# Kernel optimization log

Measured on AMD Instinct MI355X. Metric: run time of the kernel, lower is better.

Reference implementation:

```python
import jax, jax.numpy as jnp
import numpy as np

HEADS = 8
DIM = 512
DHEAD = DIM // HEADS          # 64
M_LAND = DIM // 2             # 256 landmarks
PINV_ITERS = 6
RES_K = 33                    # residual depthwise conv kernel along sequence


def _ln(x, w, b, eps=1e-5):
    mu = x.mean(-1, keepdims=True)
    var = ((x - mu) ** 2).mean(-1, keepdims=True)
    return (x - mu) * jax.lax.rsqrt(var + eps) * w + b


def _moore_penrose_pinv(x, iters=PINV_ITERS):
    # x: [b, h, m, m]; iterative Newton-Schulz style pseudo-inverse (order-3)
    abs_x = jnp.abs(x)
    col = abs_x.sum(-1).max()   # global max, matching torch.max(col)
    row = abs_x.sum(-2).max()
    z = jnp.swapaxes(x, -1, -2) / (col * row)
    I = jnp.eye(x.shape[-1], dtype=x.dtype)
    for _ in range(iters):
        xz = x @ z
        z = 0.25 * (z @ (13.0 * I - xz @ (15.0 * I - xz @ (7.0 * I - xz))))
    return z


def _nystrom_attention(x, qkv_w, out_w, out_b, res_w):
    # x: [b, n, dim]; pads at FRONT to multiple of num_landmarks
    b, n, _ = x.shape
    m = M_LAND
    pad = (m - n % m) % m
    xp = jnp.pad(x, ((0, 0), (pad, 0), (0, 0)))
    npad = n + pad
    qkv = xp @ qkv_w.T                               # [b, npad, 3*dim], no bias
    q, k, v = jnp.split(qkv, 3, axis=-1)
    heads = lambda t: t.reshape(b, npad, HEADS, DHEAD).transpose(0, 2, 1, 3)
    q, k, v = heads(q), heads(k), heads(v)           # [b, h, npad, d]
    q = q * (DHEAD ** -0.5)
    l = npad // m                                    # group size per landmark
    q_l = q.reshape(b, HEADS, m, l, DHEAD).sum(3) / l  # [b, h, m, d]
    k_l = k.reshape(b, HEADS, m, l, DHEAD).sum(3) / l
    attn1 = jax.nn.softmax(jnp.einsum('bhid,bhjd->bhij', q, k_l), -1)    # [b,h,npad,m]
    attn2 = jax.nn.softmax(jnp.einsum('bhid,bhjd->bhij', q_l, k_l), -1)  # [b,h,m,m]
    attn3 = jax.nn.softmax(jnp.einsum('bhid,bhjd->bhij', q_l, k), -1)    # [b,h,m,npad]
    attn2_inv = _moore_penrose_pinv(attn2)
    out = attn1 @ (attn2_inv @ (attn3 @ v))          # [b, h, npad, d]
    # residual depthwise conv along sequence axis (heads as channels)
    res = jax.lax.conv_general_dilated(
        v, res_w, (1, 1), ((RES_K // 2, RES_K // 2), (0, 0)),
        feature_group_count=HEADS,
        dimension_numbers=('NCHW', 'OIHW', 'NCHW'))
    out = out + res
    out = out.transpose(0, 2, 1, 3).reshape(b, npad, HEADS * DHEAD)
    out = out @ out_w.T + out_b                      # dropout = eval no-op
    return out[:, -n:]


def _translayer(x, nw, nb, qkv_w, out_w, out_b, res_w):
    return x + _nystrom_attention(_ln(x, nw, nb), qkv_w, out_w, out_b, res_w)


def _dwconv(feat, w, b, k):
    y = jax.lax.conv_general_dilated(
        feat, w, (1, 1), ((k // 2, k // 2), (k // 2, k // 2)),
        feature_group_count=DIM,
        dimension_numbers=('NCHW', 'OIHW', 'NCHW'))
    return y + b[None, :, None, None]


def _ppeg(x, w7, b7, w5, b5, w3, b3):
    B, N, C = x.shape
    H = int(np.ceil(np.sqrt(N)))   # static (N is static under jit)
    add = H * H - N
    if add > 0:
        x = jnp.concatenate([x, x[:, :add]], 1)
    feat = jnp.swapaxes(x, 1, 2).reshape(B, C, H, H)
    out = feat + _dwconv(feat, w7, b7, 7) + _dwconv(feat, w5, b5, 5) + _dwconv(feat, w3, b3, 3)
    x = jnp.swapaxes(out.reshape(B, C, H * H), 1, 2)
    if add > 0:
        x = x[:, :-add]
    return x


def setup_inputs() -> dict:
    key = jax.random.key(0)
    ks = jax.random.split(key, 24)
    B, N, C = 2, 8192, DIM
    g = lambda k, shape, s=0.02: jax.random.normal(k, shape, jnp.float32) * s
    d = {}
    d['x'] = jax.random.normal(ks[0], (B, N, C), jnp.float32)
    d['cls_token'] = jax.random.normal(ks[1], (1, 1, C), jnp.float32)
    for li, off in (('l1', 2), ('l2', 8)):
        d[li + '_norm_w'] = jnp.ones((C,), jnp.float32)
        d[li + '_norm_b'] = jnp.zeros((C,), jnp.float32)
        d[li + '_qkv_w'] = g(ks[off], (3 * C, C))
        d[li + '_out_w'] = g(ks[off + 1], (C, C))
        d[li + '_out_b'] = jnp.zeros((C,), jnp.float32)
        d[li + '_res_w'] = g(ks[off + 2], (HEADS, 1, RES_K, 1))
    d['peg_w7'] = g(ks[14], (C, 1, 7, 7)); d['peg_b7'] = jnp.zeros((C,), jnp.float32)
    d['peg_w5'] = g(ks[15], (C, 1, 5, 5)); d['peg_b5'] = jnp.zeros((C,), jnp.float32)
    d['peg_w3'] = g(ks[16], (C, 1, 3, 3)); d['peg_b3'] = jnp.zeros((C,), jnp.float32)
    d['norm_w'] = jnp.ones((C,), jnp.float32)
    d['norm_b'] = jnp.zeros((C,), jnp.float32)
    return d


def reference(x, cls_token,
              l1_norm_w, l1_norm_b, l1_qkv_w, l1_out_w, l1_out_b, l1_res_w,
              l2_norm_w, l2_norm_b, l2_qkv_w, l2_out_w, l2_out_b, l2_res_w,
              peg_w7, peg_b7, peg_w5, peg_b5, peg_w3, peg_b3,
              norm_w, norm_b):
    B = x.shape[0]
    cls = jnp.broadcast_to(cls_token, (B, 1, DIM))
    h = jnp.concatenate([cls, x], 1)
    h = _translayer(h, l1_norm_w, l1_norm_b, l1_qkv_w, l1_out_w, l1_out_b, l1_res_w)
    patches = _ppeg(h[:, 1:], peg_w7, peg_b7, peg_w5, peg_b5, peg_w3, peg_b3)
    h = jnp.concatenate([h[:, :1], patches], 1)
    h = _translayer(h, l2_norm_w, l2_norm_b, l2_qkv_w, l2_out_w, l2_out_b, l2_res_w)
    h = _ln(h, norm_w, norm_b)
    return h[:, 0]
```

## Files before the change

### kernel.cpp

```cpp
#include <hip/hip_runtime.h>
#include <hip/hip_bf16.h>

using bf16 = __hip_bfloat16;
typedef unsigned short u16;
typedef short bf16x8 __attribute__((ext_vector_type(8)));
typedef float f32x4 __attribute__((ext_vector_type(4)));

constexpr int BB    = 2;
constexpr int NSEQ  = 8193;
constexpr int CDIM  = 512;
constexpr int NH    = 8;
constexpr int DHD   = 64;
constexpr int ML    = 256;
constexpr int LF    = 33;
constexpr int NPAD  = 8448;
constexpr int PADL  = 255;
constexpr int ROWS  = BB * NSEQ;
constexpr int BH    = BB * NH;
constexpr int RKS   = 33;
constexpr int HG    = 91;
constexpr int HW2   = HG * HG;
constexpr int NPATCH = 8192;
constexpr long SQ   = (long)ML * ML;

__device__ __forceinline__ float b2f(u16 u) {
  union { unsigned int i; float f; } x; x.i = (unsigned int)u << 16; return x.f;
}
__device__ __forceinline__ short f2b(float f) {
  __hip_bfloat16 h = __float2bfloat16(f);
  return *reinterpret_cast<short*>(&h);
}
__device__ __forceinline__ f32x4 mfma16(bf16x8 a, bf16x8 b, f32x4 c) {
  return __builtin_amdgcn_mfma_f32_16x16x32_bf16(a, b, c, 0, 0, 0);
}


__global__ __launch_bounds__(256) void k_build_h(
    const float* __restrict__ x, const float* __restrict__ cls, float* __restrict__ h)
{
  long idx = (long)blockIdx.x * 256 + threadIdx.x;
  if (idx >= (long)ROWS * CDIM) return;
  int c = idx & 511;
  long r = idx >> 9;
  int b = (int)(r / NSEQ), i = (int)(r % NSEQ);
  h[idx] = (i == 0) ? cls[c] : x[((long)b * (NSEQ - 1) + (i - 1)) * CDIM + c];
}

__global__ __launch_bounds__(256) void k_cvt(
    const float* __restrict__ X, short* __restrict__ Y, long n)
{
  long i = (long)blockIdx.x * 256 + threadIdx.x;
  const long st = (long)gridDim.x * 256;
  for (; i < n; i += st) Y[i] = f2b(X[i]);
}

__global__ __launch_bounds__(256) void k_zpad(uint4* __restrict__ q)
{
  const int seg = blockIdx.y;
  const int buf = seg >> 4, bh = seg & 15;
  const long base_e = ((long)buf * BH + bh) * ((long)NPAD * DHD);
  uint4* p = (uint4*)((u16*)q + base_e);
  const int n16 = PADL * DHD * 2 / 16;
  for (int i = blockIdx.x * 256 + threadIdx.x; i < n16; i += gridDim.x * 256)
    p[i] = make_uint4(0u, 0u, 0u, 0u);
}

__global__ __launch_bounds__(256) void k_lnq(
    const float* __restrict__ X, const float* __restrict__ g,
    const float* __restrict__ bb, bf16* __restrict__ Y)
{
  __shared__ float red[4];
  const long row = blockIdx.x;
  const float* x = X + row * CDIM;
  const int t = threadIdx.x;
  float a0 = x[t], a1 = x[t + 256];
  float s = a0 + a1;
  for (int o = 32; o; o >>= 1) s += __shfl_down(s, o);
  if ((t & 63) == 0) red[t >> 6] = s;
  __syncthreads();
  const float mu = (red[0] + red[1] + red[2] + red[3]) * (1.0f / CDIM);
  __syncthreads();
  float d0 = a0 - mu, d1 = a1 - mu;
  float q = d0 * d0 + d1 * d1;
  for (int o = 32; o; o >>= 1) q += __shfl_down(q, o);
  if ((t & 63) == 0) red[t >> 6] = q;
  __syncthreads();
  const float var = (red[0] + red[1] + red[2] + red[3]) * (1.0f / CDIM);
  const float rs = rsqrtf(var + 1e-5f);
  u16* y = (u16*)Y + row * CDIM;
  y[t]       = (u16)f2b(d0 * rs * g[t]       + bb[t]);
  y[t + 256] = (u16)f2b(d1 * rs * g[t + 256] + bb[t + 256]);
}

__global__ __launch_bounds__(256) void k_final_ln(
    const float* __restrict__ H, const float* __restrict__ g,
    const float* __restrict__ bb, float* __restrict__ out)
{
  __shared__ float red[4];
  const float* x = H + (long)blockIdx.x * NSEQ * CDIM;
  const int t = threadIdx.x;
  float a0 = x[t], a1 = x[t + 256];
  float s = a0 + a1;
  for (int o = 32; o; o >>= 1) s += __shfl_down(s, o);
  if ((t & 63) == 0) red[t >> 6] = s;
  __syncthreads();
  const float mu = (red[0] + red[1] + red[2] + red[3]) * (1.0f / CDIM);
// ... 52 lines not shown
  const int t = threadIdx.x;
  float rs = 0.f, cs = 0.f;
  for (int j = 0; j < ML; ++j) { rs += fabsf(Ab[t * ML + j]); cs += fabsf(Ab[j * ML + t]); }
  for (int o = 32; o; o >>= 1) { rs = fmaxf(rs, __shfl_down(rs, o)); cs = fmaxf(cs, __shfl_down(cs, o)); }
  if ((t & 63) == 0) { r1[t >> 6] = rs; r2[t >> 6] = cs; }
  __syncthreads();
  if (t == 0) {
    red[blockIdx.x]      = fmaxf(fmaxf(r1[0], r1[1]), fmaxf(r1[2], r1[3]));
    red[16 + blockIdx.x] = fmaxf(fmaxf(r2[0], r2[1]), fmaxf(r2[2], r2[3]));
  }
}

__global__ void k_pinv_scale(float* __restrict__ red)
{
  if (threadIdx.x == 0 && blockIdx.x == 0) {
    float cmax = red[0], rmax = red[16];
    for (int i = 1; i < 16; ++i) { cmax = fmaxf(cmax, red[i]); rmax = fmaxf(rmax, red[16 + i]); }
    red[32] = 1.0f / (cmax * rmax);
  }
}

__global__ __launch_bounds__(256) void k_tscale2(
    const float* __restrict__ A, const float* __restrict__ red,
    short* __restrict__ Ab, short* __restrict__ Z, short* __restrict__ Zt)
{
  long idx = (long)blockIdx.x * 256 + threadIdx.x;
  if (idx >= (long)BH * SQ) return;
  int c = idx & 255, r = (int)((idx >> 8) & 255);
  long bh = idx >> 16;
  float a = A[idx];
  float s = red[32];
  Ab[idx] = f2b(a);
  Zt[idx] = f2b(a * s);
  Z[(bh << 16) + ((long)c << 8) + r] = f2b(a * s);
}

__global__ __launch_bounds__(256) void k_split(
    const float* __restrict__ X, float alpha, float diag,
    short* __restrict__ rH, short* __restrict__ rL,
    short* __restrict__ cH, short* __restrict__ cL)
{
  long idx = (long)blockIdx.x * 256 + threadIdx.x;
  if (idx >= (long)BH * SQ) return;
  int c = idx & 255, r = (int)((idx >> 8) & 255);
  long bh = idx >> 16;
  float v = alpha * X[idx] + ((r == c) ? diag : 0.f);
  short h = f2b(v);
  short lo = f2b(v - b2f((u16)h));
  if (rH) { rH[idx] = h; rL[idx] = lo; }
  if (cH) { long tix = (bh << 16) + ((long)c << 8) + r; cH[tix] = h; cL[tix] = lo; }
}

__global__ __launch_bounds__(256) void k_resconv2(
    const bf16* __restrict__ v, const float* __restrict__ w, bf16* __restrict__ out)
{
  __shared__ u16 vb[96][64];
  __shared__ float ws[RKS];
  const int bh = blockIdx.y, i0 = blockIdx.x * 64;
  const int t = threadIdx.x;
  if (t < RKS) ws[t] = w[(bh & 7) * RKS + t];
  const u16* vsrc = (const u16*)v + (long)bh * NPAD * DHD;
#pragma unroll
  for (int i = 0; i < 3; ++i) {
    int chunk = t + 256 * i;
    int row = chunk >> 3, c8 = (chunk & 7) * 8;
    int vrow = i0 - 16 + row;
    bf16x8 val;
    if (vrow >= 0 && vrow < NPAD) val = *(const bf16x8*)(vsrc + (long)vrow * DHD + c8);
    else { for (int j = 0; j < 8; ++j) val[j] = 0; }
    *(bf16x8*)(&vb[row][c8]) = val;
  }
  __syncthreads();
  const int d = t & 63;
  u16* ob = (u16*)out + ((long)bh * NPAD + i0) * DHD;
#pragma unroll
  for (int j = 0; j < 16; ++j) {
    int r = (t >> 6) + j * 4;
    float s = 0.f;
#pragma unroll
    for (int k = 0; k < RKS; ++k) s += b2f(vb[r + k][d]) * ws[k];
    long oi = (long)r * DHD + d;
    ob[oi] = (u16)f2b(b2f(ob[oi]) + s);
  }
}

__global__ __launch_bounds__(256) void k_vT(const bf16* __restrict__ V, bf16* __restrict__ VT)
{
  __shared__ u16 tl[64][72];
  const int r0 = blockIdx.x * 64, bh = blockIdx.y;
  const u16* vp = (const u16*)V + ((long)bh * NPAD + r0) * DHD;
  const int t = threadIdx.x;
  {
    int r = t >> 2, c0 = (t & 3) * 16;
    bf16x8 u0 = *(const bf16x8*)(vp + (long)r * DHD + c0);
    bf16x8 u1 = *(const bf16x8*)(vp + (long)r * DHD + c0 + 8);
#pragma unroll
    for (int i = 0; i < 8; ++i) { tl[r][c0 + i] = (u16)u0[i]; tl[r][c0 + 8 + i] = (u16)u1[i]; }
  }
  __syncthreads();
  {
    int d = t >> 2, k0 = (t & 3) * 16;
    bf16x8 u0, u1;
#pragma unroll
    for (int i = 0; i < 8; ++i) { u0[i] = (short)tl[k0 + i][d]; u1[i] = (short)tl[k0 + 8 + i][d]; }
    u16* dst = (u16*)VT + ((long)bh * DHD + d) * NPAD + r0 + k0;
    *(bf16x8*)dst = u0;
    *(bf16x8*)(dst + 8) = u1;
  }
}

__global__ __launch_bounds__(256) void k_t2mT(const float* __restrict__ T2M, short* __restrict__ T2MT)
{
  int idx = blockIdx.x * 256 + threadIdx.x;
  if (idx >= BH * DHD * ML) return;
  int k = idx & 255, d = (idx >> 8) & 63, bh = idx >> 14;
  T2MT[idx] = f2b(T2M[((long)bh * ML + k) * DHD + d]);
}


__global__ __launch_bounds__(256) void k_ppeg_build_t(
    const float* __restrict__ h, float* __restrict__ feat)
{
  __shared__ float tile[32][33];
  const int c0 = blockIdx.x * 32;
  const int p0 = blockIdx.y * 32;
  const int b  = blockIdx.z;
  const int t = threadIdx.x;
  const int tc = t & 31, tr8 = t >> 5;
  const int srcb = (p0 >= NPATCH) ? p0 - NPATCH : p0;
#pragma unroll
  for (int i = 0; i < 4; ++i) {
    int pp = tr8 + i * 8;
    if (p0 + pp < HW2)
      tile[pp][tc] = h[((long)b * NSEQ + 1 + srcb + pp) * CDIM + c0 + tc];
  }
  __syncthreads();
#pragma unroll
  for (int i = 0; i < 4; ++i) {
    int cc = tr8 + i * 8;
    if (p0 + tc < HW2)
      feat[((long)(b * CDIM + c0 + cc)) * HW2 + p0 + tc] = tile[tc][cc];
  }
}

__global__ __launch_bounds__(256) void k_ppeg_conv2(
    const float* __restrict__ feat,
    const float* __restrict__ w7, const float* __restrict__ b7,
    const float* __restrict__ w5, const float* __restrict__ b5,
    const float* __restrict__ w3, const float* __restrict__ b3,
    float* __restrict__ ofeat)
{
  __shared__ float P[97 * 97];
  __shared__ float ws[84];
  const int bx = blockIdx.x;
  const int c = bx & 511;
  const int t = threadIdx.x;
  for (int i = t; i < 97 * 97; i += 256) P[i] = 0.f;
  if (t < 49) ws[t] = w7[c * 49 + t];
  else if (t < 74) ws[t] = w5[c * 25 + (t - 49)];
  else if (t < 83) ws[t] = w3[c * 9 + (t - 74)];
  __syncthreads();
  const float* fp = feat + (long)bx * HW2;
  for (int i = t; i < HW2; i += 256) {
    int y = i / HG, x = i - y * HG;
    P[(y + 3) * 97 + x + 3] = fp[i];
  }
// ... 168 lines not shown
        u16* dst = (u16*)(which == 0 ? Q : (which == 1 ? Kp : V));
        dst[(((long)(b * NH + hd)) * NPAD + PADL + ii) * DHD + d] = (u16)f2b(val);
      }
    }
  }
}

__global__ __launch_bounds__(256) void k_mfma_out2(
    const bf16* __restrict__ O1, const short* __restrict__ Wm,
    const float* __restrict__ bias, float* __restrict__ Hh)
{
  __shared__ __align__(16) short As[128 * 32];
  __shared__ __align__(16) short Bs[128 * 32];
  const int m0 = blockIdx.x * 128, n0 = blockIdx.y * 128;
  const int t = threadIdx.x, w = t >> 6, l = t & 63;
  const int srow = t >> 1, skh = (t & 1) * 16;
  const int aR = m0 + srow;
  int bb = 0, ii = 0;
  if (aR < ROWS) { bb = aR / NSEQ; ii = aR - bb * NSEQ; }
  const int wR = n0 + srow;
  const int g0 = skh >> 3;
  const int sw0 = ((g0 ^ (srow & 3)) << 3), sw1 = (((g0 + 1) ^ (srow & 3)) << 3);
  const u16* o1 = (const u16*)O1;
  f32x4 acc[4][4] = {};
  for (int kt = 0; kt < 16; ++kt) {
    const int kbase = kt * 32 + skh;
    {
      bf16x8 v0, v1;
      if (aR < ROWS) {
        int hd = kbase >> 6, d0 = kbase & 63;
        const u16* src = o1 + (((long)(bb * NH + hd)) * NPAD + PADL + ii) * DHD + d0;
        v0 = *(const bf16x8*)src;
        v1 = *(const bf16x8*)(src + 8);
      } else {
#pragma unroll
        for (int i = 0; i < 8; ++i) { v0[i] = 0; v1[i] = 0; }
      }
      *(bf16x8*)(As + srow * 32 + sw0) = v0;
      *(bf16x8*)(As + srow * 32 + sw1) = v1;
    }
    {
      bf16x8 v0 = *(const bf16x8*)(Wm + (long)wR * CDIM + kbase);
      bf16x8 v1 = *(const bf16x8*)(Wm + (long)wR * CDIM + kbase + 8);
      *(bf16x8*)(Bs + srow * 32 + sw0) = v0;
      *(bf16x8*)(Bs + srow * 32 + sw1) = v1;
    }
    __syncthreads();
    const int ar0 = (w >> 1) * 64, bc0 = (w & 1) * 64;
    const int kg = l >> 4;
    bf16x8 a[4], b[4];
#pragma unroll
    for (int am = 0; am < 4; ++am) {
      int row = ar0 + am * 16 + (l & 15);
      a[am] = *(const bf16x8*)(As + row * 32 + ((kg ^ (row & 3)) << 3));
    }
#pragma unroll
    for (int bn = 0; bn < 4; ++bn) {
      int row = bc0 + bn * 16 + (l & 15);
      b[bn] = *(const bf16x8*)(Bs + row * 32 + ((kg ^ (row & 3)) << 3));
    }
#pragma unroll
    for (int am = 0; am < 4; ++am)
#pragma unroll
      for (int bn = 0; bn < 4; ++bn) acc[am][bn] = mfma16(a[am], b[bn], acc[am][bn]);
    __syncthreads();
  }
  const int ar0 = (w >> 1) * 64, bc0 = (w & 1) * 64;
#pragma unroll
  for (int am = 0; am < 4; ++am) {
#pragma unroll
    for (int rr = 0; rr < 4; ++rr) {
      int R = m0 + ar0 + am * 16 + ((l >> 4) << 2) + rr;
      if (R >= ROWS) continue;
      float* hrow = Hh + (long)R * CDIM;
#pragma unroll
      for (int bn = 0; bn < 4; ++bn) {
        int n = n0 + bc0 + bn * 16 + (l & 15);
        hrow[n] += acc[am][bn][rr] + bias[n];
      }
    }
  }
}


__global__ __launch_bounds__(256) void k_pinv_g(
    const short* __restrict__ A, const short* __restrict__ Bt,
    short* __restrict__ outN, float aN, float dN,
    short* __restrict__ outT, float aT, float dT,
    float* __restrict__ outF, float aF)
{
  const int bh = blockIdx.z;
  const long off = (long)bh * SQ;
  const short* Ab = A + off;
  const short* Btb = Bt + off;
  const int t = threadIdx.x, w = t >> 6, l = t & 63;
  const int r0 = blockIdx.x * 64 + (w >> 1) * 32;
  const int c0 = blockIdx.y * 64 + (w & 1) * 32;
  f32x4 acc[2][2] = {};
#pragma unroll
  for (int ks = 0; ks < 8; ++ks) {
    bf16x8 a[2], b[2];
#pragma unroll
    for (int am = 0; am < 2; ++am)
      a[am] = *(const bf16x8*)(Ab + (long)(r0 + am * 16 + (l & 15)) * ML + ks * 32 + (l >> 4) * 8);
#pragma unroll
    for (int bn = 0; bn < 2; ++bn)
      b[bn] = *(const bf16x8*)(Btb + (long)(c0 + bn * 16 + (l & 15)) * ML + ks * 32 + (l >> 4) * 8);
#pragma unroll
    for (int am = 0; am < 2; ++am)
#pragma unroll
      for (int bn = 0; bn < 2; ++bn) acc[am][bn] = mfma16(a[am], b[bn], acc[am][bn]);
  }
#pragma unroll
  for (int am = 0; am < 2; ++am)
#pragma unroll
    for (int bn = 0; bn < 2; ++bn)
#pragma unroll
      for (int rr = 0; rr < 4; ++rr) {
        int R = r0 + am * 16 + ((l >> 4) << 2) + rr;
        int C = c0 + bn * 16 + (l & 15);
        float x = acc[am][bn][rr];
        float dg = (R == C) ? 1.f : 0.f;
        if (outN) outN[off + (long)R * ML + C] = f2b(aN * x + dN * dg);
        if (outT) outT[off + (long)C * ML + R] = f2b(aT * x + dT * dg);
        if (outF) outF[off + (long)R * ML + C] = aF * x;
      }
}

__global__ __launch_bounds__(256) void k_pinv_gs(
    const short* __restrict__ Ah, const short* __restrict__ Al,
    const short* __restrict__ BhT, const short* __restrict__ BlT,
    float* __restrict__ outF, float alpha, float diag)
{
  const int bh = blockIdx.z;
  const long off = (long)bh * SQ;
  const int t = threadIdx.x, w = t >> 6, l = t & 63;
  const int r0 = blockIdx.x * 64 + (w >> 1) * 32;
  const int c0 = blockIdx.y * 64 + (w & 1) * 32;
  f32x4 acc[2][2] = {};
#pragma unroll
  for (int ks = 0; ks < 8; ++ks) {
    bf16x8 ah[2], al[2], bh_[2], bl[2];
#pragma unroll
    for (int am = 0; am < 2; ++am) {
      long base = off + (long)(r0 + am * 16 + (l & 15)) * ML + ks * 32 + (l >> 4) * 8;
      ah[am] = *(const bf16x8*)(Ah + base);
      al[am] = *(const bf16x8*)(Al + base);
    }
#pragma unroll
    for (int bn = 0; bn < 2; ++bn) {
      long base = off + (long)(c0 + bn * 16 + (l & 15)) * ML + ks * 32 + (l >> 4) * 8;
      bh_[bn] = *(const bf16x8*)(BhT + base);
      bl[bn] = *(const bf16x8*)(BlT + base);
    }
#pragma unroll
    for (int am = 0; am < 2; ++am)
#pragma unroll
      for (int bn = 0; bn < 2; ++bn) {
        acc[am][bn] = mfma16(ah[am], bh_[bn], acc[am][bn]);
        acc[am][bn] = mfma16(ah[am], bl[bn], acc[am][bn]);
        acc[am][bn] = mfma16(al[am], bh_[bn], acc[am][bn]);
      }
  }
#pragma unroll
  for (int am = 0; am < 2; ++am)
#pragma unroll
    for (int bn = 0; bn < 2; ++bn)
#pragma unroll
      for (int rr = 0; rr < 4; ++rr) {
        int R = r0 + am * 16 + ((l >> 4) << 2) + rr;
        int C = c0 + bn * 16 + (l & 15);
        float y = alpha * acc[am][bn][rr];
        if (R == C) y += diag;
        outF[off + (long)R * ML + C] = y;
      }
}

__global__ __launch_bounds__(256) void k_score_g(
    const bf16* __restrict__ A, const bf16* __restrict__ Bt, float* __restrict__ C)
{
  const int bh = blockIdx.z;
  const u16* Ab = (const u16*)A + (long)bh * ML * DHD;
  const u16* Btb = (const u16*)Bt + (long)bh * ML * DHD;
  float* Cb = C + (long)bh * SQ;
  const int t = threadIdx.x, w = t >> 6, l = t & 63;
  const int r0 = blockIdx.x * 64 + (w >> 1) * 32;
  const int c0 = blockIdx.y * 64 + (w & 1) * 32;
  f32x4 acc[2][2] = {};
#pragma unroll
  for (int ks = 0; ks < 2; ++ks) {
    bf16x8 a[2], b[2];
#pragma unroll
    for (int am = 0; am < 2; ++am)
      a[am] = *(const bf16x8*)(Ab + (long)(r0 + am * 16 + (l & 15)) * DHD + ks * 32 + (l >> 4) * 8);
#pragma unroll
    for (int bn = 0; bn < 2; ++bn)
      b[bn] = *(const bf16x8*)(Btb + (long)(c0 + bn * 16 + (l & 15)) * DHD + ks * 32 + (l >> 4) * 8);
#pragma unroll
    for (int am = 0; am < 2; ++am)
#pragma unroll
      for (int bn = 0; bn < 2; ++bn) acc[am][bn] = mfma16(a[am], b[bn], acc[am][bn]);
  }
#pragma unroll
  for (int am = 0; am < 2; ++am)
#pragma unroll
    for (int bn = 0; bn < 2; ++bn)
#pragma unroll
      for (int rr = 0; rr < 4; ++rr) {
        int R = r0 + am * 16 + ((l >> 4) << 2) + rr;
        int Cc = c0 + bn * 16 + (l & 15);
        Cb[(long)R * ML + Cc] = acc[am][bn][rr];
      }
}


__device__ __forceinline__ int pswz(int row, int col) {
  return row * 256 + ((((col >> 3) ^ (row & 7)) << 3) | (col & 7));
}

__global__ __launch_bounds__(256) void k_attn3(
    const bf16* __restrict__ QL, const bf16* __restrict__ Kb,
    const bf16* __restrict__ VT, float* __restrict__ T3V)
{
  __shared__ __align__(16) u16 Pl[64 * 256];
  __shared__ float psum[4][64];
  __shared__ float lsum[64];
  const int bh = blockIdx.y;
  const int m0 = blockIdx.x * 64;
  const int t = threadIdx.x, w = t >> 6, l = t & 63;
  const u16* qlp = (const u16*)QL + (long)bh * ML * DHD;
  const u16* kp  = (const u16*)Kb + (long)bh * NPAD * DHD;
  const u16* vtp = (const u16*)VT + (long)bh * DHD * NPAD;

  bf16x8 a[4][2];
#pragma unroll
  for (int am = 0; am < 4; ++am)
#pragma unroll
    for (int ks = 0; ks < 2; ++ks)
      a[am][ks] = *(const bf16x8*)(qlp + (long)(m0 + am * 16 + (l & 15)) * DHD + ks * 32 + (l >> 4) * 8);

  float p_[16];
#pragma unroll
  for (int i = 0; i < 16; ++i) p_[i] = 0.f;
  f32x4 o[4][4] = {};

  for (int kt = 0; kt < NPAD / 256; ++kt) {
    const int kv0 = kt * 256 + w * 64;
    f32x4 s[4][4] = {};
#pragma unroll
    for (int ks = 0; ks < 2; ++ks)
#pragma unroll
      for (int bc = 0; bc < 4; ++bc) {
        bf16x8 bbv = *(const bf16x8*)(kp + (long)(kv0 + bc * 16 + (l & 15)) * DHD + ks * 32 + (l >> 4) * 8);
#pragma unroll
        for (int am = 0; am < 4; ++am) s[am][bc] = mfma16(a[am][ks], bbv, s[am][bc]);
      }
#pragma unroll
    for (int am = 0; am < 4; ++am)
#pragma unroll
      for (int bc = 0; bc < 4; ++bc)
#pragma unroll
        for (int rr = 0; rr < 4; ++rr) {
          float e = __expf(s[am][bc][rr]);
          p_[am * 4 + rr] += e;
          Pl[pswz(am * 16 + ((l >> 4) << 2) + rr, w * 64 + bc * 16 + (l & 15))] = (u16)f2b(e);
        }
    __syncthreads();
#pragma unroll
    for (int ks = 0; ks < 2; ++ks) {
      bf16x8 pa[4];
#pragma unroll
      for (int am = 0; am < 4; ++am)
        pa[am] = *(const bf16x8*)(Pl + pswz(am * 16 + (l & 15), w * 64 + ks * 32 + (l >> 4) * 8));
#pragma unroll
      for (int dn = 0; dn < 4; ++dn) {
        bf16x8 vb = *(const bf16x8*)(vtp + (long)(dn * 16 + (l & 15)) * NPAD + kt * 256 + w * 64 + ks * 32 + (l >> 4) * 8);
#pragma unroll
        for (int am = 0; am < 4; ++am) o[am][dn] = mfma16(pa[am], vb, o[am][dn]);
      }
    }
    __syncthreads();
  }
#pragma unroll
  for (int i = 0; i < 16; ++i) {
    float v = p_[i];
    v += __shfl_xor(v, 1); v += __shfl_xor(v, 2); v += __shfl_xor(v, 4); v += __shfl_xor(v, 8);
    p_[i] = v;
  }
  if ((l & 15) == 0) {
#pragma unroll
    for (int am = 0; am < 4; ++am)
#pragma unroll
      for (int rr = 0; rr < 4; ++rr)
        psum[w][am * 16 + ((l >> 4) << 2) + rr] = p_[am * 4 + rr];
  }
  __syncthreads();
  if (t < 64) lsum[t] = psum[0][t] + psum[1][t] + psum[2][t] + psum[3][t];
  __syncthreads();

  float* Obuf = (float*)Pl;
  for (int wv = 0; wv < 4; ++wv) {
    if (w == wv) {
#pragma unroll
      for (int am = 0; am < 4; ++am)
#pragma unroll
        for (int dn = 0; dn < 4; ++dn)
#pragma unroll
          for (int rr = 0; rr < 4; ++rr) {
            int row = am * 16 + ((l >> 4) << 2) + rr, col = dn * 16 + (l & 15);
            if (wv == 0) Obuf[row * 64 + col] = o[am][dn][rr];
            else         Obuf[row * 64 + col] += o[am][dn][rr];
          }
    }
    __syncthreads();
  }
  {
    int row = t >> 2, c0 = (t & 3) * 16;
    float inv = 1.0f / lsum[row];
    float* dst = T3V + ((long)bh * ML + m0 + row) * DHD + c0;
#pragma unroll
    for (int i = 0; i < 16; ++i) dst[i] = Obuf[row * 64 + c0 + i] * inv;
  }
}

__global__ __launch_bounds__(256) void k_attn1(
    const bf16* __restrict__ Qb, const bf16* __restrict__ KL,
    const short* __restrict__ T2MT, bf16* __restrict__ O1)
{
  __shared__ __align__(16) u16 Pl[64 * 256];
  __shared__ float psum[4][64];
  __shared__ float lsum[64];
  const int bh = blockIdx.y;
  const int m0 = blockIdx.x * 64;
  const int t = threadIdx.x, w = t >> 6, l = t & 63;
  const u16* qp  = (const u16*)Qb + (long)bh * NPAD * DHD;
  const u16* klp = (const u16*)KL + (long)bh * ML * DHD;
  const short* tp = T2MT + (long)bh * DHD * ML;

  bf16x8 a[4][2];
#pragma unroll
  for (int am = 0; am < 4; ++am)
#pragma unroll
    for (int ks = 0; ks < 2; ++ks)
      a[am][ks] = *(const bf16x8*)(qp + (long)(m0 + am * 16 + (l & 15)) * DHD + ks * 32 + (l >> 4) * 8);

  f32x4 s[4][4] = {};
#pragma unroll
  for (int ks = 0; ks < 2; ++ks)
#pragma unroll
    for (int bc = 0; bc < 4; ++bc) {
      bf16x8 bbv = *(const bf16x8*)(klp + (long)(w * 64 + bc * 16 + (l & 15)) * DHD + ks * 32 + (l >> 4) * 8);
#pragma unroll
      for (int am = 0; am < 4; ++am) s[am][bc] = mfma16(a[am][ks], bbv, s[am][bc]);
    }
  float p_[16];
#pragma unroll
  for (int am = 0; am < 4; ++am)
#pragma unroll
    for (int rr = 0; rr < 4; ++rr)
      p_[am * 4 + rr] = __expf(s[am][0][rr]) + __expf(s[am][1][rr])
                      + __expf(s[am][2][rr]) + __expf(s[am][3][rr]);
#pragma unroll
  for (int i = 0; i < 16; ++i) {
    float v = p_[i];
    v += __shfl_xor(v, 1); v += __shfl_xor(v, 2); v += __shfl_xor(v, 4); v += __shfl_xor(v, 8);
    p_[i] = v;
  }
  if ((l & 15) == 0) {
#pragma unroll
    for (int am = 0; am < 4; ++am)
#pragma unroll
      for (int rr = 0; rr < 4; ++rr)
        psum[w][am * 16 + ((l >> 4) << 2) + rr] = p_[am * 4 + rr];
  }
#pragma unroll
  for (int am = 0; am < 4; ++am)
#pragma unroll
    for (int bc = 0; bc < 4; ++bc)
#pragma unroll
      for (int rr = 0; rr < 4; ++rr)
        Pl[pswz(am * 16 + ((l >> 4) << 2) + rr, w * 64 + bc * 16 + (l & 15))] =
            (u16)f2b(__expf(s[am][bc][rr]));
  __syncthreads();
  if (t < 64) lsum[t] = psum[0][t] + psum[1][t] + psum[2][t] + psum[3][t];
  __syncthreads();

  f32x4 o[4][4] = {};
#pragma unroll
  for (int ks = 0; ks < 2; ++ks) {
    bf16x8 pa[4];
#pragma unroll
    for (int am = 0; am < 4; ++am)
      pa[am] = *(const bf16x8*)(Pl + pswz(am * 16 + (l & 15), w * 64 + ks * 32 + (l >> 4) * 8));
#pragma unroll
    for (int dn = 0; dn < 4; ++dn) {
      bf16x8 vb = *(const bf16x8*)((const u16*)tp + (long)(dn * 16 + (l & 15)) * ML + w * 64 + ks * 32 + (l >> 4) * 8);
#pragma unroll
      for (int am = 0; am < 4; ++am) o[am][dn] = mfma16(pa[am], vb, o[am][dn]);
    }
  }
  float* Obuf = (float*)Pl;
  __syncthreads();
  for (int wv = 0; wv < 4; ++wv) {
    if (w == wv) {
#pragma unroll
      for (int am = 0; am < 4; ++am)
#pragma unroll
        for (int dn = 0; dn < 4; ++dn)
#pragma unroll
          for (int rr = 0; rr < 4; ++rr) {
            int row = am * 16 + ((l >> 4) << 2) + rr, col = dn * 16 + (l & 15);
            if (wv == 0) Obuf[row * 64 + col] = o[am][dn][rr];
            else         Obuf[row * 64 + col] += o[am][dn][rr];
          }
    }
    __syncthreads();
  }
  {
    int row = t >> 2, c0 = (t & 3) * 16;
    float inv = 1.0f / lsum[row];
    u16* dst = (u16*)O1 + ((long)bh * NPAD + m0 + row) * DHD + c0;
    bf16x8 r0, r1;
#pragma unroll
    for (int i = 0; i < 8; ++i) {
      r0[i] = f2b(Obuf[row * 64 + c0 + i] * inv);
      r1[i] = f2b(Obuf[row * 64 + c0 + 8 + i] * inv);
    }
    *(bf16x8*)dst = r0;
    *(bf16x8*)(dst + 8) = r1;
  }
}


struct WSP {
  float *h, *a2, *Za, *t3v, *t2m, *red;
  bf16 *q, *k, *v, *vT, *ql, *kl, *lnq;
  short *pu, *wqb, *wob, *t2mT;
  short *Ab, *Zc, *Zt, *Z2, *Z2t, *xz, *w1t, *w2t;
};

static void run_translayer(const float* nw, const float* nb, const float* qkvw,
                           const float* outw, const float* outb, const float* resw,
                           WSP& w, hipStream_t s)
{
  const size_t S2 = (size_t)BH * SQ;
  short* U = w.pu;

  k_cvt<<<768, 256, 0, s>>>(qkvw, w.wqb, (long)3 * CDIM * CDIM);
  k_cvt<<<256, 256, 0, s>>>(outw, w.wob, (long)CDIM * CDIM);
  k_lnq<<<ROWS, 256, 0, s>>>(w.h, nw, nb, w.lnq);
  k_zpad<<<dim3(8, 48), 256, 0, s>>>((uint4*)w.q);
  k_mfma_qkv2<<<dim3(129, 12), 256, 0, s>>>(w.lnq, w.wqb, w.q, w.k, w.v);
  k_vT<<<dim3(NPAD / 64, BH), 256, 0, s>>>(w.v, w.vT);

  const int lmN = BH * ML * DHD;
  k_landmark<<<(lmN + 255) / 256, 256, 0, s>>>(w.q, w.ql);
  k_landmark<<<(lmN + 255) / 256, 256, 0, s>>>(w.k, w.kl);

  k_score_g<<<dim3(4, 4, BH), 256, 0, s>>>(w.ql, w.kl, w.a2);
  k_softmax<<<BH * ML, 256, 0, s>>>(w.a2, ML);
  k_pinv_prep<<<BH, 256, 0, s>>>(w.a2, w.red);
  k_pinv_scale<<<1, 64, 0, s>>>(w.red);

  k_attn3<<<dim3(4, BH), 256, 0, s>>>(w.ql, w.k, w.vT, w.t3v);

  const long nz = (long)BH * SQ;
  const int sg = (int)((nz + 255) / 256);
  k_tscale2<<<sg, 256, 0, s>>>(w.a2, w.red, w.Ab, w.Zc, w.Zt);
  short *Zc = w.Zc, *Zt = w.Zt, *Z2 = w.Z2, *Z2t = w.Z2t;
  for (int it = 0; it < 5; ++it) {
    k_pinv_g<<<dim3(4, 4, BH), 256, 0, s>>>(w.Ab, Zt, w.xz, 1.f, 0.f, w.w1t, -1.f, 7.f, nullptr, 0.f);
    k_pinv_g<<<dim3(4, 4, BH), 256, 0, s>>>(w.xz, w.w1t, nullptr, 0.f, 0.f, w.w2t, -1.f, 15.f, nullptr, 0.f);
    k_pinv_g<<<dim3(4, 4, BH), 256, 0, s>>>(w.xz, w.w2t, nullptr, 0.f, 0.f, w.w1t, -1.f, 13.f, nullptr, 0.f);
    k_pinv_g<<<dim3(4, 4, BH), 256, 0, s>>>(Zc, w.w1t, Z2, 0.25f, 0.f, Z2t, 0.25f, 0.f,
                                            (it == 4) ? w.Za : nullptr, 0.25f);
    short* tm;
    tm = Zc; Zc = Z2; Z2 = tm;
    tm = Zt; Zt = Z2t; Z2t = tm;
  }
  float* T0f = (float*)(U + 4 * S2);
  float* Tf2 = (float*)(U + 2 * S2);
  k_split<<<sg, 256, 0, s>>>(w.a2, 1.f, 0.f, U + 0 * S2, U + 1 * S2, nullptr, nullptr);
  k_split<<<sg, 256, 0, s>>>(w.Za, 1.f, 0.f, nullptr, nullptr, U + 2 * S2, U + 3 * S2);
  k_pinv_gs<<<dim3(4, 4, BH), 256, 0, s>>>(U + 0 * S2, U + 1 * S2, U + 2 * S2, U + 3 * S2, T0f, 1.f, 0.f);
  k_split<<<sg, 256, 0, s>>>(T0f, -1.f, 7.f, nullptr, nullptr, U + 6 * S2, U + 7 * S2);
  k_split<<<sg, 256, 0, s>>>(T0f, 1.f, 0.f, U + 0 * S2, U + 1 * S2, nullptr, nullptr);
  k_pinv_gs<<<dim3(4, 4, BH), 256, 0, s>>>(U + 0 * S2, U + 1 * S2, U + 6 * S2, U + 7 * S2, Tf2, 1.f, 0.f);
  k_split<<<sg, 256, 0, s>>>(Tf2, -1.f, 15.f, nullptr, nullptr, U + 6 * S2, U + 7 * S2);
  k_pinv_gs<<<dim3(4, 4, BH), 256, 0, s>>>(U + 0 * S2, U + 1 * S2, U + 6 * S2, U + 7 * S2, Tf2, 1.f, 0.f);
  k_split<<<sg, 256, 0, s>>>(Tf2, -1.f, 13.f, nullptr, nullptr, U + 4 * S2, U + 5 * S2);
  k_split<<<sg, 256, 0, s>>>(w.Za, 1.f, 0.f, U + 6 * S2, U + 7 * S2, nullptr, nullptr);
  k_pinv_gs<<<dim3(4, 4, BH), 256, 0, s>>>(U + 6 * S2, U + 7 * S2, U + 4 * S2, U + 5 * S2, w.Za, 0.25f, 0.f);

  k_gemm_nn<<<dim3(4, 1, BH), 256, 0, s>>>(w.Za, w.t3v, w.t2m, ML, DHD, ML,
                                           SQ, (long)ML * DHD, (long)ML * DHD, 1.f, 0.f);
  k_t2mT<<<(BH * DHD * ML + 255) / 256, 256, 0, s>>>(w.t2m, w.t2mT);

  k_attn1<<<dim3(NPAD / 64, BH), 256, 0, s>>>(w.q, w.kl, w.t2mT, w.q);

  k_resconv2<<<dim3(NPAD / 64, BH), 256, 0, s>>>(w.v, resw, w.q);

  k_mfma_out2<<<dim3(129, 4), 256, 0, s>>>(w.q, w.wob, outb, w.h);
}

extern "C" void kernel_launch(void* const* d_in, const int* in_sizes, int n_in,
                              void* d_out, int out_size, void* d_ws, size_t ws_size,
                              hipStream_t stream)
{
  const float* x      = (const float*)d_in[0];
  const float* cls    = (const float*)d_in[1];
  const float* l1nw   = (const float*)d_in[2];
  const float* l1nb   = (const float*)d_in[3];
  const float* l1qkvw = (const float*)d_in[4];
  const float* l1outw = (const float*)d_in[5];
  const float* l1outb = (const float*)d_in[6];
  const float* l1resw = (const float*)d_in[7];
  const float* l2nw   = (const float*)d_in[8];
  const float* l2nb   = (const float*)d_in[9];
  const float* l2qkvw = (const float*)d_in[10];
  const float* l2outw = (const float*)d_in[11];
  const float* l2outb = (const float*)d_in[12];
  const float* l2resw = (const float*)d_in[13];
  const float* pw7    = (const float*)d_in[14];
  const float* pb7    = (const float*)d_in[15];
  const float* pw5    = (const float*)d_in[16];
  const float* pb5    = (const float*)d_in[17];
  const float* pw3    = (const float*)d_in[18];
  const float* pb3    = (const float*)d_in[19];
  const float* fnw    = (const float*)d_in[20];
  const float* fnb    = (const float*)d_in[21];
  (void)in_sizes; (void)n_in; (void)out_size; (void)ws_size;

  float* W = (float*)d_ws;
  size_t o = 0;
  auto alloc = [&](size_t n) { float* p = W + o; o += n; return p; };
  WSP w;
  w.h = alloc((size_t)ROWS * CDIM);
  float* qkvr = alloc((size_t)3 * BH * NPAD * DHD / 2);
  w.q = (bf16*)qkvr;
  w.k = w.q + (size_t)BH * NPAD * DHD;
  w.v = w.k + (size_t)BH * NPAD * DHD;
  float* vtr = alloc((size_t)BH * NPAD * DHD / 2);
  w.vT  = (bf16*)vtr;
  w.lnq = (bf16*)vtr;
  w.pu  = (short*)vtr;
  {
    const size_t S2 = (size_t)BH * SQ;
    w.Ab = w.pu;             w.Zc  = w.pu + S2;     w.Zt  = w.pu + 2 * S2; w.Z2 = w.pu + 3 * S2;
    w.Z2t = w.pu + 4 * S2;   w.xz  = w.pu + 5 * S2; w.w1t = w.pu + 6 * S2; w.w2t = w.pu + 7 * S2;
  }
  float* wbr = alloc((size_t)(3 * CDIM * CDIM + CDIM * CDIM) / 2);
  w.wqb = (short*)wbr;
  w.wob = w.wqb + (size_t)3 * CDIM * CDIM;
  float* lmr = alloc((size_t)2 * BH * ML * DHD / 2);
  w.ql = (bf16*)lmr;
  w.kl = w.ql + (size_t)BH * ML * DHD;
  w.a2  = alloc((size_t)BH * SQ);
  w.Za  = alloc((size_t)BH * SQ);
  w.t3v = alloc((size_t)BH * ML * DHD);
  w.t2m = alloc((size_t)BH * ML * DHD);
  float* ttr = alloc((size_t)BH * ML * DHD / 2);
  w.t2mT = (short*)ttr;
  w.red = alloc(64);

  const long nh = (long)ROWS * CDIM;
  k_build_h<<<(int)((nh + 255) / 256), 256, 0, stream>>>(x, cls, w.h);

  run_translayer(l1nw, l1nb, l1qkvw, l1outw, l1outb, l1resw, w, stream);

  float* feat  = (float*)w.q;
  float* ofeat = (float*)w.v;
  k_ppeg_build_t<<<dim3(16, 259, BB), 256, 0, stream>>>(w.h, feat);
  k_ppeg_conv2<<<BB * CDIM, 256, 0, stream>>>(feat, pw7, pb7, pw5, pb5, pw3, pb3, ofeat);
  k_ppeg_scat_t<<<dim3(16, 256, BB), 256, 0, stream>>>(ofeat, w.h);

  run_translayer(l2nw, l2nb, l2qkvw, l2outw, l2outb, l2resw, w, stream);

  k_final_ln<<<BB, 256, 0, stream>>>(w.h, fnw, fnb, (float*)d_out);
}
```

Before: 1.712 ms.

## Split-K attn3 across sequence and compute only the cls row in layer two

The attn3 landmark-to-sequence attention is split across four sequence chunks with more, smaller blocks, and a separate reduction kernel combines the partial outputs and sums. This raises parallelism beyond the previous 64 blocks. In the second transformer layer only the cls row's output is needed for the final result, so attn1, the residual conv and the output projection are replaced by single-row kernels. This skips most of the full-sequence work and is valid because only h[:,0] is returned. The cost is extra scratch traffic for the partials, which reuse the Za buffer.

```diff
diff --git a/kernel.cpp b/kernel.cpp
--- a/kernel.cpp
+++ b/kernel.cpp
@@ -22,6 +22,8 @@
 constexpr int HW2   = HG * HG;
 constexpr int NPATCH = 8192;
 constexpr long SQ   = (long)ML * ML;
+constexpr int KSPLIT = 4;
+constexpr int NKT   = NPAD / 256;
 
 __device__ __forceinline__ float b2f(u16 u) {
   union { unsigned int i; float f; } x; x.i = (unsigned int)u << 16; return x.f;
@@ -240,6 +242,24 @@
     long oi = (long)r * DHD + d;
     ob[oi] = (u16)f2b(b2f(ob[oi]) + s);
   }
+}
+
+__global__ __launch_bounds__(256) void k_resconv_r0(
+    const bf16* __restrict__ v, const float* __restrict__ w, bf16* __restrict__ out)
+{
+  int idx = blockIdx.x * 256 + threadIdx.x;
+  if (idx >= BH * DHD) return;
+  int bh = idx >> 6, d = idx & 63;
+  const float* wp = w + (bh & 7) * RKS;
+  const u16* vb = (const u16*)v + (long)bh * NPAD * DHD + d;
+  float s = 0.f;
+#pragma unroll
+  for (int t = 0; t < RKS; ++t) {
+    int src = PADL + t - 16;
+    s += b2f(vb[(long)src * DHD]) * wp[t];
+  }
+  u16* ob = (u16*)out + ((long)bh * NPAD + PADL) * DHD + d;
+  *ob = (u16)f2b(b2f(*ob) + s);
 }
 
 __global__ __launch_bounds__(256) void k_vT(const bf16* __restrict__ V, bf16* __restrict__ VT)
@@ -574,6 +594,23 @@
   }
 }
 
+__global__ __launch_bounds__(256) void k_out_r0(
+    const bf16* __restrict__ O1, const short* __restrict__ Wm,
+    const float* __restrict__ bias, float* __restrict__ Hh)
+{
+  __shared__ float mrow[CDIM];
+  const int b = blockIdx.x, t = threadIdx.x;
+  for (int c = t; c < CDIM; c += 256)
+    mrow[c] = b2f(((const u16*)O1)[(((long)(b * NH + (c >> 6))) * NPAD + PADL) * DHD + (c & 63)]);
+  __syncthreads();
+  for (int n = t; n < CDIM; n += 256) {
+    float s = 0.f;
+    const u16* wr = (const u16*)Wm + (long)n * CDIM;
+    for (int k = 0; k < CDIM; ++k) s += mrow[k] * b2f(wr[k]);
+    Hh[(long)b * NSEQ * CDIM + n] += s + bias[n];
+  }
+}
+
 
 __global__ __launch_bounds__(256) void k_pinv_g(
     const short* __restrict__ A, const short* __restrict__ Bt,
@@ -710,91 +747,93 @@
   return row * 256 + ((((col >> 3) ^ (row & 7)) << 3) | (col & 7));
 }
 
-__global__ __launch_bounds__(256) void k_attn3(
+__global__ __launch_bounds__(256) void k_attn3s(
     const bf16* __restrict__ QL, const bf16* __restrict__ Kb,
-    const bf16* __restrict__ VT, float* __restrict__ T3V)
-{
-  __shared__ __align__(16) u16 Pl[64 * 256];
-  __shared__ float psum[4][64];
-  __shared__ float lsum[64];
-  const int bh = blockIdx.y;
-  const int m0 = blockIdx.x * 64;
+    const bf16* __restrict__ VT, float* __restrict__ po, float* __restrict__ pl)
+{
+  __shared__ __align__(16) u16 Pl[32 * 256];
+  __shared__ float psum[4][32];
+  __shared__ float lsum[32];
+  const int bh = blockIdx.z;
+  const int m0 = blockIdx.x * 32;
+  const int s  = blockIdx.y;
+  const int kt0 = (NKT * s) / KSPLIT, kt1 = (NKT * (s + 1)) / KSPLIT;
   const int t = threadIdx.x, w = t >> 6, l = t & 63;
   const u16* qlp = (const u16*)QL + (long)bh * ML * DHD;
   const u16* kp  = (const u16*)Kb + (long)bh * NPAD * DHD;
   const u16* vtp = (const u16*)VT + (long)bh * DHD * NPAD;
 
-  bf16x8 a[4][2];
-#pragma unroll
-  for (int am = 0; am < 4; ++am)
+  bf16x8 a[2][2];
+#pragma unroll
+  for (int am = 0; am < 2; ++am)
 #pragma unroll
     for (int ks = 0; ks < 2; ++ks)
       a[am][ks] = *(const bf16x8*)(qlp + (long)(m0 + am * 16 + (l & 15)) * DHD + ks * 32 + (l >> 4) * 8);
 
-  float p_[16];
-#pragma unroll
-  for (int i = 0; i < 16; ++i) p_[i] = 0.f;
-  f32x4 o[4][4] = {};
-
-  for (int kt = 0; kt < NPAD / 256; ++kt) {
+  float p_[8];
+#pragma unroll
+  for (int i = 0; i < 8; ++i) p_[i] = 0.f;
+  f32x4 o[2][4] = {};
+
+  for (int kt = kt0; kt < kt1; ++kt) {
     const int kv0 = kt * 256 + w * 64;
-    f32x4 s[4][4] = {};
+    f32x4 sa[2][4] = {};
 #pragma unroll
     for (int ks = 0; ks < 2; ++ks)
 #pragma unroll
       for (int bc = 0; bc < 4; ++bc) {
         bf16x8 bbv = *(const bf16x8*)(kp + (long)(kv0 + bc * 16 + (l & 15)) * DHD + ks * 32 + (l >> 4) * 8);
 #pragma unroll
-        for (int am = 0; am < 4; ++am) s[am][bc] = mfma16(a[am][ks], bbv, s[am][bc]);
+        for (int am = 0; am < 2; ++am) sa[am][bc] = mfma16(a[am][ks], bbv, sa[am][bc]);
       }
 #pragma unroll
-    for (int am = 0; am < 4; ++am)
+    for (int am = 0; am < 2; ++am)
 #pragma unroll
       for (int bc = 0; bc < 4; ++bc)
 #pragma unroll
         for (int rr = 0; rr < 4; ++rr) {
-          float e = __expf(s[am][bc][rr]);
+          float e = __expf(sa[am][bc][rr]);
           p_[am * 4 + rr] += e;
           Pl[pswz(am * 16 + ((l >> 4) << 2) + rr, w * 64 + bc * 16 + (l & 15))] = (u16)f2b(e);
         }
     __syncthreads();
 #pragma unroll
     for (int ks = 0; ks < 2; ++ks) {
-      bf16x8 pa[4];
-#pragma unroll
-      for (int am = 0; am < 4; ++am)
+      bf16x8 pa[2];
+#pragma unroll
+      for (int am = 0; am < 2; ++am)
         pa[am] = *(const bf16x8*)(Pl + pswz(am * 16 + (l & 15), w * 64 + ks * 32 + (l >> 4) * 8));
 #pragma unroll
       for (int dn = 0; dn < 4; ++dn) {
         bf16x8 vb = *(const bf16x8*)(vtp + (long)(dn * 16 + (l & 15)) * NPAD + kt * 256 + w * 64 + ks * 32 + (l >> 4) * 8);
 #pragma unroll
-        for (int am = 0; am < 4; ++am) o[am][dn] = mfma16(pa[am], vb, o[am][dn]);
+        for (int am = 0; am < 2; ++am) o[am][dn] = mfma16(pa[am], vb, o[am][dn]);
       }
     }
     __syncthreads();
   }
 #pragma unroll
-  for (int i = 0; i < 16; ++i) {
+  for (int i = 0; i < 8; ++i) {
     float v = p_[i];
     v += __shfl_xor(v, 1); v += __shfl_xor(v, 2); v += __shfl_xor(v, 4); v += __shfl_xor(v, 8);
     p_[i] = v;
   }
   if ((l & 15) == 0) {
 #pragma unroll
-    for (int am = 0; am < 4; ++am)
+    for (int am = 0; am < 2; ++am)
 #pragma unroll
       for (int rr = 0; rr < 4; ++rr)
         psum[w][am * 16 + ((l >> 4) << 2) + rr] = p_[am * 4 + rr];
   }
   __syncthreads();
-  if (t < 64) lsum[t] = psum[0][t] + psum[1][t] + psum[2][t] + psum[3][t];
+  if (t < 32) lsum[t] = psum[0][t] + psum[1][t] + psum[2][t] + psum[3][t];
   __syncthreads();
 
   float* Obuf = (float*)Pl;
   for (int wv = 0; wv < 4; ++wv) {
     if (w == wv) {
 #pragma unroll
-      for (int am = 0; am < 4; ++am)
+      for (int am = 0; am < 2; ++am)
 #pragma unroll
         for (int dn = 0; dn < 4; ++dn)
 #pragma unroll
@@ -806,13 +845,30 @@
     }
     __syncthreads();
   }
-  {
-    int row = t >> 2, c0 = (t & 3) * 16;
-    float inv = 1.0f / lsum[row];
-    float* dst = T3V + ((long)bh * ML + m0 + row) * DHD + c0;
-#pragma unroll
-    for (int i = 0; i < 16; ++i) dst[i] = Obuf[row * 64 + c0 + i] * inv;
-  }
+  const long pbase = (long)(bh * 8 + blockIdx.x) * KSPLIT + s;
+#pragma unroll
+  for (int i = 0; i < 8; ++i) {
+    int idx2 = t * 8 + i;
+    po[pbase * 2048 + idx2] = Obuf[idx2];
+  }
+  if (t < 32) pl[pbase * 32 + t] = lsum[t];
+}
+
+__global__ __launch_bounds__(256) void k_attn3r(
+    const float* __restrict__ po, const float* __restrict__ pl, float* __restrict__ T3V)
+{
+  int idx = blockIdx.x * 256 + threadIdx.x;
+  if (idx >= BH * ML * DHD) return;
+  int d = idx & 63, row = (idx >> 6) & 255, bh = idx >> 14;
+  int mb = row >> 5, r = row & 31;
+  long p0 = (long)(bh * 8 + mb) * KSPLIT;
+  float o = 0.f, ll = 0.f;
+#pragma unroll
+  for (int s = 0; s < KSPLIT; ++s) {
+    o  += po[(p0 + s) * 2048 + r * 64 + d];
+    ll += pl[(p0 + s) * 32 + r];
+  }
+  T3V[idx] = o / ll;
 }
 
 __global__ __launch_bounds__(256) void k_attn1(
@@ -923,9 +979,43 @@
   }
 }
 
+__global__ __launch_bounds__(256) void k_attn1_r0(
+    const bf16* __restrict__ Qb, const bf16* __restrict__ KL,
+    const float* __restrict__ T2M, bf16* __restrict__ O1)
+{
+  __shared__ float qrow[DHD];
+  __shared__ float p[ML];
+  __shared__ float red[4];
+  __shared__ float ored[4][DHD];
+  const int bh = blockIdx.x, t = threadIdx.x;
+  const u16* qp = (const u16*)Qb + ((long)bh * NPAD + PADL) * DHD;
+  if (t < DHD) qrow[t] = b2f(qp[t]);
+  __syncthreads();
+  const u16* klp = (const u16*)KL + (long)bh * ML * DHD;
+  float sj = 0.f;
+  for (int d = 0; d < DHD; ++d) sj += qrow[d] * b2f(klp[t * DHD + d]);
+  float e = __expf(sj);
+  p[t] = e;
+  float sum = e;
+  for (int o = 32; o; o >>= 1) sum += __shfl_down(sum, o);
+  if ((t & 63) == 0) red[t >> 6] = sum;
+  __syncthreads();
+  const float inv = 1.0f / (red[0] + red[1] + red[2] + red[3]);
+  const float* tm = T2M + (long)bh * ML * DHD;
+  const int part = t >> 6, d = t & 63;
+  float acc = 0.f;
+  for (int j = part * 64; j < part * 64 + 64; ++j) acc += p[j] * tm[(long)j * DHD + d];
+  ored[part][d] = acc;
+  __syncthreads();
+  if (t < DHD) {
+    float v = (ored[0][t] + ored[1][t] + ored[2][t] + ored[3][t]) * inv;
+    ((u16*)O1)[((long)bh * NPAD + PADL) * DHD + t] = (u16)f2b(v);
+  }
+}
+
 
 struct WSP {
-  float *h, *a2, *Za, *t3v, *t2m, *red;
+  float *h, *a2, *Za, *t3v, *t2m, *red, *pl;
   bf16 *q, *k, *v, *vT, *ql, *kl, *lnq;
   short *pu, *wqb, *wob, *t2mT;
   short *Ab, *Zc, *Zt, *Z2, *Z2t, *xz, *w1t, *w2t;
@@ -933,7 +1023,7 @@
 
 static void run_translayer(const float* nw, const float* nb, const float* qkvw,
                            const float* outw, const float* outb, const float* resw,
-                           WSP& w, hipStream_t s)
+                           WSP& w, hipStream_t s, bool row0)
 {
   const size_t S2 = (size_t)BH * SQ;
   short* U = w.pu;
@@ -954,7 +1044,8 @@
   k_pinv_prep<<<BH, 256, 0, s>>>(w.a2, w.red);
   k_pinv_scale<<<1, 64, 0, s>>>(w.red);
 
-  k_attn3<<<dim3(4, BH), 256, 0, s>>>(w.ql, w.k, w.vT, w.t3v);
+  k_attn3s<<<dim3(8, KSPLIT, BH), 256, 0, s>>>(w.ql, w.k, w.vT, w.Za, w.pl);
+  k_attn3r<<<(BH * ML * DHD + 255) / 256, 256, 0, s>>>(w.Za, w.pl, w.t3v);
 
   const long nz = (long)BH * SQ;
   const int sg = (int)((nz + 255) / 256);
@@ -986,13 +1077,17 @@
 
   k_gemm_nn<<<dim3(4, 1, BH), 256, 0, s>>>(w.Za, w.t3v, w.t2m, ML, DHD, ML,
                                            SQ, (long)ML * DHD, (long)ML * DHD, 1.f, 0.f);
-  k_t2mT<<<(BH * DHD * ML + 255) / 256, 256, 0, s>>>(w.t2m, w.t2mT);
-
-  k_attn1<<<dim3(NPAD / 64, BH), 256, 0, s>>>(w.q, w.kl, w.t2mT, w.q);
-
-  k_resconv2<<<dim3(NPAD / 64, BH), 256, 0, s>>>(w.v, resw, w.q);
-
-  k_mfma_out2<<<dim3(129, 4), 256, 0, s>>>(w.q, w.wob, outb, w.h);
+
+  if (!row0) {
+    k_t2mT<<<(BH * DHD * ML + 255) / 256, 256, 0, s>>>(w.t2m, w.t2mT);
+    k_attn1<<<dim3(NPAD / 64, BH), 256, 0, s>>>(w.q, w.kl, w.t2mT, w.q);
+    k_resconv2<<<dim3(NPAD / 64, BH), 256, 0, s>>>(w.v, resw, w.q);
+    k_mfma_out2<<<dim3(129, 4), 256, 0, s>>>(w.q, w.wob, outb, w.h);
+  } else {
+    k_attn1_r0<<<BH, 256, 0, s>>>(w.q, w.kl, w.t2m, w.q);
+    k_resconv_r0<<<(BH * DHD + 255) / 256, 256, 0, s>>>(w.v, resw, w.q);
+    k_out_r0<<<BB, 256, 0, s>>>(w.q, w.wob, outb, w.h);
+  }
 }
 
 extern "C" void kernel_launch(void* const* d_in, const int* in_sizes, int n_in,
@@ -1053,12 +1148,13 @@
   w.t2m = alloc((size_t)BH * ML * DHD);
   float* ttr = alloc((size_t)BH * ML * DHD / 2);
   w.t2mT = (short*)ttr;
+  w.pl  = alloc((size_t)BH * 8 * KSPLIT * 32);
   w.red = alloc(64);
 
   const long nh = (long)ROWS * CDIM;
   k_build_h<<<(int)((nh + 255) / 256), 256, 0, stream>>>(x, cls, w.h);
 
-  run_translayer(l1nw, l1nb, l1qkvw, l1outw, l1outb, l1resw, w, stream);
+  run_translayer(l1nw, l1nb, l1qkvw, l1outw, l1outb, l1resw, w, stream, false);
 
   float* feat  = (float*)w.q;
   float* ofeat = (float*)w.v;
@@ -1066,7 +1162,7 @@
   k_ppeg_conv2<<<BB * CDIM, 256, 0, stream>>>(feat, pw7, pb7, pw5, pb5, pw3, pb3, ofeat);
   k_ppeg_scat_t<<<dim3(16, 256, BB), 256, 0, stream>>>(ofeat, w.h);
 
-  run_translayer(l2nw, l2nb, l2qkvw, l2outw, l2outb, l2resw, w, stream);
+  run_translayer(l2nw, l2nb, l2qkvw, l2outw, l2outb, l2resw, w, stream, true);
 
   k_final_ln<<<BB, 256, 0, stream>>>(w.h, fnw, fnb, (float*)d_out);
 }
```

After: 1.394 ms. -18.6%, faster.
